# Kernel optimization log

Hardware: AMD Instinct MI355X
Metric: run time of the kernel (lower is better)

## Reference

```python
import jax, jax.numpy as jnp
import numpy as np

D, J, K, H = 4, 256, 512, 512  # d, num_output, num_input, num_hidden
B = 1024


def setup_inputs() -> dict:
    key = jax.random.key(0)
    ks = jax.random.split(key, 8)
    x = jax.random.normal(ks[0], (B, K), dtype=jnp.float32)
    # self.w = ((1-0.1)*U + 0.1) / num_input, shape [d, num_output, num_input]
    w = ((0.9 * jax.random.uniform(ks[1], (D, J, K), dtype=jnp.float32) + 0.1) / K)
    # Stacked per-output-MLP params (nn.Linear default init scale 1/sqrt(fan_in))
    s0 = 1.0 / np.sqrt(K)
    s1 = 1.0 / np.sqrt(H)
    W0 = jax.random.uniform(ks[2], (J, H, K), dtype=jnp.float32, minval=-s0, maxval=s0)
    b0 = jax.random.uniform(ks[3], (J, H), dtype=jnp.float32, minval=-s0, maxval=s0)
    W1 = jax.random.uniform(ks[4], (J, H), dtype=jnp.float32, minval=-s1, maxval=s1)  # [J,1,H] squeezed
    b1 = jax.random.uniform(ks[5], (J,), dtype=jnp.float32, minval=-s1, maxval=s1)
    logvar = jnp.ones((D,), dtype=jnp.float32) * -4.0
    return {"x": x, "i": 0, "w": w, "W0": W0, "b0": b0, "W1": W1, "b1": b1, "logvar": logvar}


def reference(x, i, w, W0, b0, W1, b1, logvar):
    # For each output j: mu[:, j] = lin1_j(LeakyReLU(lin0_j(w[i, j] * x)))
    # Fused as a single grouped GEMM over j: fold the mask w[i] into the contraction.
    wi = w[i]                                   # [J, K]
    h = jnp.einsum('jhk,jk,bk->bjh', W0, wi, x) + b0[None, :, :]   # [B, J, H]
    h = jax.nn.leaky_relu(h, negative_slope=0.01)
    mu = jnp.einsum('bjh,jh->bj', h, W1) + b1[None, :]             # [B, J]
    return (mu, logvar)
```

## Files before the change

kernel.cpp:

```cpp
#include <hip/hip_runtime.h>

#define J_ 256
#define K_ 512
#define H_ 512
#define B_ 1024

typedef float f32x4 __attribute__((ext_vector_type(4)));
typedef unsigned int u32x4 __attribute__((ext_vector_type(4)));
typedef unsigned short u16x4 __attribute__((ext_vector_type(4)));
typedef unsigned short u16x8 __attribute__((ext_vector_type(8)));
typedef __bf16 bf16x8 __attribute__((ext_vector_type(8)));

__device__ __forceinline__ unsigned short f2bf(float f) {
    unsigned int u = __float_as_uint(f);
    u += 0x7fffu + ((u >> 16) & 1u);
    return (unsigned short)(u >> 16);
}

__device__ __forceinline__ void gload_lds16(const void* g, void* l) {
    __builtin_amdgcn_global_load_lds(
        (const __attribute__((address_space(1))) unsigned int*)g,
        (__attribute__((address_space(3))) unsigned int*)l, 16, 0, 0);
}

__global__ __launch_bounds__(256) void prep_kernel(
    const float* __restrict__ x, const float* __restrict__ b1,
    const float* __restrict__ logvar, unsigned short* __restrict__ xbf,
    float* __restrict__ out) {
    int t = blockIdx.x * 256 + threadIdx.x;
    {
        f32x4 v = *(const f32x4*)(x + (size_t)t * 4);
        u16x4 o;
        o[0] = f2bf(v[0]); o[1] = f2bf(v[1]); o[2] = f2bf(v[2]); o[3] = f2bf(v[3]);
        *(u16x4*)(xbf + (size_t)t * 4) = o;
    }
    if (t < (B_ * J_) / 4) {
        int b = t >> 6;
        int j4 = (t & 63) << 2;
        f32x4 bb = *(const f32x4*)(b1 + j4);
        *(f32x4*)(out + ((size_t)b << 8) + j4) = bb;
    }
    if (t < 4) out[B_ * J_ + t] = logvar[t];
}

__global__ __launch_bounds__(256) void wprep_kernel(
    const float* __restrict__ W0, const float* __restrict__ wmask,
    const int* __restrict__ ip, unsigned short* __restrict__ w0p) {
    size_t t = (size_t)blockIdx.x * 256 + threadIdx.x;
    size_t e = t * 8;
    int j = (int)(e >> 18);
    int k = (int)(e & (K_ - 1));
    const float* wi = wmask + ((size_t)ip[0] * J_ + j) * K_ + k;
    f32x4 s0 = *(const f32x4*)wi;
    f32x4 s1 = *(const f32x4*)(wi + 4);
    f32x4 a0 = *(const f32x4*)(W0 + e);
    f32x4 a1 = *(const f32x4*)(W0 + e + 4);
    a0 *= s0; a1 *= s1;
    u16x8 o;
    #pragma unroll
    for (int q = 0; q < 4; ++q) { o[q] = f2bf(a0[q]); o[q + 4] = f2bf(a1[q]); }
    *(u16x8*)(w0p + e) = o;
}

__global__ __launch_bounds__(512, 1) void enc_kernel(
    const unsigned short* __restrict__ xbf,
    const unsigned short* __restrict__ w0p,
    const float* __restrict__ b0,
    const float* __restrict__ W1,
    float* __restrict__ out) {
    __shared__ unsigned char lds[3 * 49152];

    int p = blockIdx.x;
    int xcd = p & 7;
    int q = p >> 3;
    int j = (xcd << 5) + (q >> 4);
    int inner = q & 15;
    int m0 = (inner >> 2) << 8;
    int h0 = (inner & 3) << 7;

    int tid = threadIdx.x;
    int lane = tid & 63;
    int wv = tid >> 6;
    int wmv = wv >> 1;
    int wnv = wv & 1;
    int lr = lane & 15, lg = lane >> 4;

    int lrow = lane >> 3;
    int lch = lane & 7;
    int sch = ((lch ^ lrow) << 3);

    const unsigned short* aSrc = xbf + (size_t)(m0 + wv * 8 + lrow) * K_ + sch;
    const unsigned short* bSrc = w0p + ((size_t)j * H_ + h0 + wv * 8 + lrow) * K_ + sch;
    unsigned char* ldsAW = lds + wv * 1024;
    unsigned char* ldsBW = lds + 32768 + wv * 1024;

    f32x4 acc[4][4] = {};

#define VMW(n) do { asm volatile("s_waitcnt vmcnt(" #n ")" ::: "memory"); \
                    __builtin_amdgcn_sched_barrier(0); } while (0)
#define BAR() do { __builtin_amdgcn_s_barrier(); \
                   __builtin_amdgcn_sched_barrier(0); } while (0)

#define STAGE(bi, ks) do { \
    _Pragma("unroll") for (int ii = 0; ii < 4; ++ii) \
        gload_lds16(aSrc + (size_t)ii * 64 * K_ + (ks) * 64, \
                    ldsAW + (bi) * 49152 + ii * 8192); \
    _Pragma("unroll") for (int ii = 0; ii < 2; ++ii) \
        gload_lds16(bSrc + (size_t)ii * 64 * K_ + (ks) * 64, \
                    ldsBW + (bi) * 49152 + ii * 8192); \
    } while (0)

#define COMPUTE(bi) do { \
    const unsigned char* LA = lds + (bi) * 49152; \
    const unsigned char* LB = LA + 32768; \
    _Pragma("unroll") for (int kf = 0; kf < 2; ++kf) { \
        bf16x8 af[4], bv[4]; \
        int colk = (kf << 6) + (lg << 4); \
        _Pragma("unroll") for (int mf = 0; mf < 4; ++mf) { \
            int r = (wmv << 6) + (mf << 4) + lr; \
            af[mf] = *(const bf16x8*)(LA + r * 128 + (colk ^ ((r & 7) << 4))); \
        } \
        _Pragma("unroll") for (int nf = 0; nf < 4; ++nf) { \
            int hr = (wnv << 6) + (nf << 4) + lr; \
            bv[nf] = *(const bf16x8*)(LB + hr * 128 + (colk ^ ((hr & 7) << 4))); \
        } \
        __builtin_amdgcn_s_setprio(1); \
        _Pragma("unroll") for (int mf = 0; mf < 4; ++mf) \
            _Pragma("unroll") for (int nf = 0; nf < 4; ++nf) \
                acc[mf][nf] = __builtin_amdgcn_mfma_f32_16x16x32_bf16( \
                    af[mf], bv[nf], acc[mf][nf], 0, 0, 0); \
        __builtin_amdgcn_s_setprio(0); \
    } } while (0)

    STAGE(0, 0); STAGE(1, 1);
    STAGE(2, 2); VMW(12); BAR(); COMPUTE(0); BAR();
    STAGE(0, 3); VMW(12); BAR(); COMPUTE(1); BAR();
    STAGE(1, 4); VMW(12); BAR(); COMPUTE(2); BAR();
    STAGE(2, 5); VMW(12); BAR(); COMPUTE(0); BAR();
    STAGE(0, 6); VMW(12); BAR(); COMPUTE(1); BAR();
    STAGE(1, 7); VMW(12); BAR(); COMPUTE(2); BAR();
                 VMW(6);  BAR(); COMPUTE(0); BAR();
                 VMW(0);  BAR(); COMPUTE(1);

    float b0v[4], w1v[4];
    #pragma unroll
    for (int nf = 0; nf < 4; ++nf) {
        int col = h0 + (wnv << 6) + (nf << 4) + lr;
        b0v[nf] = b0[(size_t)j * H_ + col];
        w1v[nf] = W1[(size_t)j * H_ + col];
    }
    #pragma unroll
    for (int mf = 0; mf < 4; ++mf) {
        #pragma unroll
        for (int rg = 0; rg < 4; ++rg) {
            float ps = 0.f;
            #pragma unroll
            for (int nf = 0; nf < 4; ++nf) {
                float hv = acc[mf][nf][rg] + b0v[nf];
                hv = hv > 0.f ? hv : 0.01f * hv;
                ps += hv * w1v[nf];
            }
            ps += __shfl_xor(ps, 1);
            ps += __shfl_xor(ps, 2);
            ps += __shfl_xor(ps, 4);
            ps += __shfl_xor(ps, 8);
            if (lr == 0) {
                int row = m0 + (wmv << 6) + (mf << 4) + (lg << 2) + rg;
                atomicAdd(out + (size_t)row * J_ + j, ps);
            }
        }
    }
#undef VMW
#undef BAR
#undef STAGE
#undef COMPUTE
}

__global__ __launch_bounds__(256, 2) void enc_kernel_fb(
    const unsigned short* __restrict__ xbf,
    const float* __restrict__ W0,
    const float* __restrict__ wmask,
    const int* __restrict__ ip,
    const float* __restrict__ b0,
    const float* __restrict__ W1,
    float* __restrict__ out) {
    __shared__ unsigned char ldsA[128 * 128];
    __shared__ unsigned char ldsB[128 * 128];

    int p = blockIdx.x;
    int xcd = p & 7;
    int q = p >> 3;
    int j = (xcd << 5) + (q >> 5);
    int inner = q & 31;
    int m0 = (inner >> 2) << 7;
    int h0 = (inner & 3) << 7;

    int i = ip[0];
    const float* w0j = W0 + (size_t)j * (H_ * K_);
    const float* wij = wmask + ((size_t)i * J_ + j) * K_;

    int tid = threadIdx.x;
    int lane = tid & 63;
    int wv = tid >> 6;
    int wm = wv >> 1, wn = wv & 1;
    int lr = lane & 15, lg = lane >> 4;
    int srow0 = tid >> 3;
    int c = tid & 7;

    f32x4 acc[4][4] = {};

    for (int ks = 0; ks < K_ / 64; ++ks) {
        int k0 = ks * 64;
        #pragma unroll
        for (int it = 0; it < 4; ++it) {
            int r = srow0 + it * 32;
            u32x4 v = *(const u32x4*)(xbf + (size_t)(m0 + r) * K_ + k0 + c * 8);
            *(u32x4*)(ldsA + r * 128 + ((c * 16) ^ ((r & 7) << 4))) = v;
        }
        f32x4 s0 = *(const f32x4*)(wij + k0 + c * 8);
        f32x4 s1 = *(const f32x4*)(wij + k0 + c * 8 + 4);
        #pragma unroll
        for (int it = 0; it < 4; ++it) {
            int hr = srow0 + it * 32;
            const float* src = w0j + (size_t)(h0 + hr) * K_ + k0 + c * 8;
            f32x4 a0 = *(const f32x4*)(src);
            f32x4 a1 = *(const f32x4*)(src + 4);
            a0 *= s0; a1 *= s1;
            u16x8 bvv;
            #pragma unroll
            for (int e = 0; e < 4; ++e) { bvv[e] = f2bf(a0[e]); bvv[e + 4] = f2bf(a1[e]); }
            *(u16x8*)(ldsB + hr * 128 + ((c * 16) ^ ((hr & 7) << 4))) = bvv;
        }
        __syncthreads();
        #pragma unroll
        for (int kf = 0; kf < 2; ++kf) {
            bf16x8 af[4], bfr[4];
            #pragma unroll
            for (int mf = 0; mf < 4; ++mf) {
                int r = (wm << 6) + (mf << 4) + lr;
                af[mf] = *(const bf16x8*)(ldsA + r * 128 +
                          (((kf << 6) + (lg << 4)) ^ ((r & 7) << 4)));
            }
            #pragma unroll
            for (int nf = 0; nf < 4; ++nf) {
                int hrw = (wn << 6) + (nf << 4) + lr;
                bfr[nf] = *(const bf16x8*)(ldsB + hrw * 128 +
                          (((kf << 6) + (lg << 4)) ^ ((hrw & 7) << 4)));
            }
            #pragma unroll
            for (int mf = 0; mf < 4; ++mf)
                #pragma unroll
                for (int nf = 0; nf < 4; ++nf)
                    acc[mf][nf] = __builtin_amdgcn_mfma_f32_16x16x32_bf16(
                        af[mf], bfr[nf], acc[mf][nf], 0, 0, 0);
        }
        __syncthreads();
    }

    float b0v[4], w1v[4];
    #pragma unroll
    for (int nf = 0; nf < 4; ++nf) {
        int h = h0 + (wn << 6) + (nf << 4) + lr;
        b0v[nf] = b0[(size_t)j * H_ + h];
        w1v[nf] = W1[(size_t)j * H_ + h];
    }
    #pragma unroll
    for (int mf = 0; mf < 4; ++mf) {
        #pragma unroll
        for (int rg = 0; rg < 4; ++rg) {
            float ps = 0.f;
            #pragma unroll
            for (int nf = 0; nf < 4; ++nf) {
                float hv = acc[mf][nf][rg] + b0v[nf];
                hv = hv > 0.f ? hv : 0.01f * hv;
                ps += hv * w1v[nf];
            }
            ps += __shfl_xor(ps, 1);
            ps += __shfl_xor(ps, 2);
            ps += __shfl_xor(ps, 4);
            ps += __shfl_xor(ps, 8);
            if (lr == 0) {
                int row = m0 + (wm << 6) + (mf << 4) + (lg << 2) + rg;
                atomicAdd(out + (size_t)row * J_ + j, ps);
            }
        }
    }
}

extern "C" void kernel_launch(void* const* d_in, const int* in_sizes, int n_in,
                              void* d_out, int out_size, void* d_ws, size_t ws_size,
                              hipStream_t stream) {
    const float* x      = (const float*)d_in[0];
    const int*   ip     = (const int*)d_in[1];
    const float* wmask  = (const float*)d_in[2];
    const float* W0     = (const float*)d_in[3];
    const float* b0     = (const float*)d_in[4];
    const float* W1     = (const float*)d_in[5];
    const float* b1     = (const float*)d_in[6];
    const float* logvar = (const float*)d_in[7];
    float* out = (float*)d_out;
    unsigned short* xbf = (unsigned short*)d_ws;
    const size_t xbf_elems = (size_t)B_ * K_;
    const size_t w0p_bytes = (size_t)J_ * H_ * K_ * 2;
    const size_t need = xbf_elems * 2 + w0p_bytes;

    prep_kernel<<<512, 256, 0, stream>>>(x, b1, logvar, xbf, out);
    if (ws_size >= need) {
        unsigned short* w0p = xbf + xbf_elems;
        wprep_kernel<<<32768, 256, 0, stream>>>(W0, wmask, ip, w0p);
        enc_kernel<<<4096, 512, 0, stream>>>(xbf, w0p, b0, W1, out);
    } else {
        enc_kernel_fb<<<8192, 256, 0, stream>>>(xbf, W0, wmask, ip, b0, W1, out);
    }
}
```

Before: 587.0 us.

## Enlarge GEMM tile to 256x256 with 4-stage K32 pipeline and register prefetch

Restructures the grouped GEMM kernel so each block computes a 256x256 tile (8 waves arranged 2x4) instead of 256x128, halving the grid. It also cuts the K-step to 32 with a 4-deep LDS ring (128 KB instead of 144 KB) and a new swizzle. LDS fragments for the next step are prefetched into registers while MFMAs run, and the A and B staging loads are split around mid-iteration barriers. The larger tile raises arithmetic intensity and halves the atomic partial sums, but it doubles accumulator registers and requests 2 blocks per CU, which may not fit in LDS and can cause register spills.

After: 596.3 us. No clear change (+1.6%).

```diff
diff --git a/kernel.cpp b/kernel.cpp
--- a/kernel.cpp
+++ b/kernel.cpp
@@ -62,85 +62,102 @@
     *(u16x8*)(w0p + e) = o;
 }
 
-__global__ __launch_bounds__(512, 1) void enc_kernel(
+__global__ __launch_bounds__(512, 2) void enc_kernel(
     const unsigned short* __restrict__ xbf,
     const unsigned short* __restrict__ w0p,
     const float* __restrict__ b0,
     const float* __restrict__ W1,
     float* __restrict__ out) {
-    __shared__ unsigned char lds[3 * 49152];
+    __shared__ unsigned char ldsA[4 * 16384];
+    __shared__ unsigned char ldsB[4 * 16384];
 
     int p = blockIdx.x;
     int xcd = p & 7;
-    int q = p >> 3;
-    int j = (xcd << 5) + (q >> 4);
-    int inner = q & 15;
-    int m0 = (inner >> 2) << 8;
-    int h0 = (inner & 3) << 7;
+    int t = p >> 3;
+    int j = (xcd << 5) + (t >> 3);
+    int inner = t & 7;
+    int m0 = (inner >> 1) << 8;
+    int h0 = (inner & 1) << 8;
 
     int tid = threadIdx.x;
     int lane = tid & 63;
     int wv = tid >> 6;
-    int wmv = wv >> 1;
-    int wnv = wv & 1;
+    int wmv = wv >> 2;
+    int wnv = wv & 3;
     int lr = lane & 15, lg = lane >> 4;
 
-    int lrow = lane >> 3;
-    int lch = lane & 7;
-    int sch = ((lch ^ lrow) << 3);
-
-    const unsigned short* aSrc = xbf + (size_t)(m0 + wv * 8 + lrow) * K_ + sch;
-    const unsigned short* bSrc = w0p + ((size_t)j * H_ + h0 + wv * 8 + lrow) * K_ + sch;
-    unsigned char* ldsAW = lds + wv * 1024;
-    unsigned char* ldsBW = lds + 32768 + wv * 1024;
-
-    f32x4 acc[4][4] = {};
+    int sRow = lane >> 2;
+    int sChk = lane & 3;
+    int srcChunk = sChk ^ ((lane >> 3) & 3);
+
+    const unsigned short* aSrc = xbf + (size_t)(m0 + wv * 16 + sRow) * K_ + srcChunk * 8;
+    const unsigned short* bSrc = w0p + ((size_t)j * H_ + h0 + wv * 16 + sRow) * K_ + srcChunk * 8;
+    unsigned char* ldsAw = ldsA + wv * 1024;
+    unsigned char* ldsBw = ldsB + wv * 1024;
+
+    int fx = (lg ^ ((lr >> 1) & 3)) << 4;
+    const unsigned char* aF = ldsA + (wmv * 128 + lr) * 64 + fx;
+    const unsigned char* bF = ldsB + (wnv * 64 + lr) * 64 + fx;
+
+    f32x4 acc[8][4] = {};
 
 #define VMW(n) do { asm volatile("s_waitcnt vmcnt(" #n ")" ::: "memory"); \
                     __builtin_amdgcn_sched_barrier(0); } while (0)
+#define LGKM0() do { asm volatile("s_waitcnt lgkmcnt(0)" ::: "memory"); \
+                     __builtin_amdgcn_sched_barrier(0); } while (0)
 #define BAR() do { __builtin_amdgcn_s_barrier(); \
                    __builtin_amdgcn_sched_barrier(0); } while (0)
-
-#define STAGE(bi, ks) do { \
-    _Pragma("unroll") for (int ii = 0; ii < 4; ++ii) \
-        gload_lds16(aSrc + (size_t)ii * 64 * K_ + (ks) * 64, \
-                    ldsAW + (bi) * 49152 + ii * 8192); \
-    _Pragma("unroll") for (int ii = 0; ii < 2; ++ii) \
-        gload_lds16(bSrc + (size_t)ii * 64 * K_ + (ks) * 64, \
-                    ldsBW + (bi) * 49152 + ii * 8192); \
-    } while (0)
-
-#define COMPUTE(bi) do { \
-    const unsigned char* LA = lds + (bi) * 49152; \
-    const unsigned char* LB = LA + 32768; \
-    _Pragma("unroll") for (int kf = 0; kf < 2; ++kf) { \
-        bf16x8 af[4], bv[4]; \
-        int colk = (kf << 6) + (lg << 4); \
-        _Pragma("unroll") for (int mf = 0; mf < 4; ++mf) { \
-            int r = (wmv << 6) + (mf << 4) + lr; \
-            af[mf] = *(const bf16x8*)(LA + r * 128 + (colk ^ ((r & 7) << 4))); \
-        } \
-        _Pragma("unroll") for (int nf = 0; nf < 4; ++nf) { \
-            int hr = (wnv << 6) + (nf << 4) + lr; \
-            bv[nf] = *(const bf16x8*)(LB + hr * 128 + (colk ^ ((hr & 7) << 4))); \
-        } \
-        __builtin_amdgcn_s_setprio(1); \
-        _Pragma("unroll") for (int mf = 0; mf < 4; ++mf) \
-            _Pragma("unroll") for (int nf = 0; nf < 4; ++nf) \
-                acc[mf][nf] = __builtin_amdgcn_mfma_f32_16x16x32_bf16( \
-                    af[mf], bv[nf], acc[mf][nf], 0, 0, 0); \
-        __builtin_amdgcn_s_setprio(0); \
-    } } while (0)
-
-    STAGE(0, 0); STAGE(1, 1);
-    STAGE(2, 2); VMW(12); BAR(); COMPUTE(0); BAR();
-    STAGE(0, 3); VMW(12); BAR(); COMPUTE(1); BAR();
-    STAGE(1, 4); VMW(12); BAR(); COMPUTE(2); BAR();
-    STAGE(2, 5); VMW(12); BAR(); COMPUTE(0); BAR();
-    STAGE(0, 6); VMW(12); BAR(); COMPUTE(1); BAR();
-    STAGE(1, 7); VMW(12); BAR(); COMPUTE(2); BAR();
-                 VMW(6);  BAR(); COMPUTE(0); BAR();
-                 VMW(0);  BAR(); COMPUTE(1);
+#define STG_A(tt) do { int c_ = (tt) & 3; \
+    gload_lds16(aSrc + (tt) * 32,                      ldsAw + c_ * 16384); \
+    gload_lds16(aSrc + (tt) * 32 + (size_t)128 * K_,   ldsAw + c_ * 16384 + 8192); } while (0)
+#define STG_B(tt) do { int c_ = (tt) & 3; \
+    gload_lds16(bSrc + (tt) * 32,                      ldsBw + c_ * 16384); \
+    gload_lds16(bSrc + (tt) * 32 + (size_t)128 * K_,   ldsBw + c_ * 16384 + 8192); } while (0)
+#define LD_A(dst, tt, mf) (dst) = *(const bf16x8*)(aF + ((tt) & 3) * 16384 + (mf) * 1024)
+#define LD_B(dst, tt, nf) (dst) = *(const bf16x8*)(bF + ((tt) & 3) * 16384 + (nf) * 1024)
+#define MFMAQ(mq, ar) do { __builtin_amdgcn_s_setprio(1); \
+    _Pragma("unroll") for (int nf_ = 0; nf_ < 4; ++nf_) { \
+      _Pragma("unroll") for (int mf_ = 0; mf_ < 4; ++mf_) \
+        acc[(mq) * 4 + mf_][nf_] = __builtin_amdgcn_mfma_f32_16x16x32_bf16( \
+            ar[mf_], bC[nf_], acc[(mq) * 4 + mf_][nf_], 0, 0, 0); } \
+    __builtin_amdgcn_s_setprio(0); } while (0)
+
+    STG_A(0); STG_B(0); STG_A(1); STG_B(1); STG_A(2); STG_B(2);
+    VMW(8);
+    BAR();
+
+    bf16x8 aLo[4], bC[4];
+    LD_A(aLo[0], 0, 0); LD_A(aLo[1], 0, 1); LD_A(aLo[2], 0, 2); LD_A(aLo[3], 0, 3);
+    LD_B(bC[0], 0, 0);  LD_B(bC[1], 0, 1);  LD_B(bC[2], 0, 2);  LD_B(bC[3], 0, 3);
+
+    #pragma unroll
+    for (int kt = 0; kt < 16; ++kt) {
+        if (kt <= 12) STG_A(kt + 3);
+        bf16x8 aHi[4];
+        LD_A(aHi[0], kt, 4); LD_A(aHi[1], kt, 5);
+        LD_A(aHi[2], kt, 6); LD_A(aHi[3], kt, 7);
+        MFMAQ(0, aLo);
+        LGKM0();
+        if (kt <= 12)      { VMW(6); }
+        else if (kt == 13) { VMW(4); }
+        else if (kt == 14) { VMW(0); }
+        BAR();
+        if (kt <= 12) STG_B(kt + 3);
+        bf16x8 aN[4], bN[4];
+        if (kt < 15) {
+            LD_A(aN[0], kt + 1, 0); LD_A(aN[1], kt + 1, 1);
+            LD_A(aN[2], kt + 1, 2); LD_A(aN[3], kt + 1, 3);
+            LD_B(bN[0], kt + 1, 0); LD_B(bN[1], kt + 1, 1);
+            LD_B(bN[2], kt + 1, 2); LD_B(bN[3], kt + 1, 3);
+        }
+        MFMAQ(1, aHi);
+        if (kt < 15) {
+            LGKM0();
+            BAR();
+            aLo[0] = aN[0]; aLo[1] = aN[1]; aLo[2] = aN[2]; aLo[3] = aN[3];
+            bC[0] = bN[0];  bC[1] = bN[1];  bC[2] = bN[2];  bC[3] = bN[3];
+        }
+    }
 
     float b0v[4], w1v[4];
     #pragma unroll
@@ -150,7 +167,7 @@
         w1v[nf] = W1[(size_t)j * H_ + col];
     }
     #pragma unroll
-    for (int mf = 0; mf < 4; ++mf) {
+    for (int mf = 0; mf < 8; ++mf) {
         #pragma unroll
         for (int rg = 0; rg < 4; ++rg) {
             float ps = 0.f;
@@ -165,15 +182,19 @@
             ps += __shfl_xor(ps, 4);
             ps += __shfl_xor(ps, 8);
             if (lr == 0) {
-                int row = m0 + (wmv << 6) + (mf << 4) + (lg << 2) + rg;
+                int row = m0 + (wmv << 7) + (mf << 4) + (lg << 2) + rg;
                 atomicAdd(out + (size_t)row * J_ + j, ps);
             }
         }
     }
 #undef VMW
+#undef LGKM0
 #undef BAR
-#undef STAGE
-#undef COMPUTE
+#undef STG_A
+#undef STG_B
+#undef LD_A
+#undef LD_B
+#undef MFMAQ
 }
 
 __global__ __launch_bounds__(256, 2) void enc_kernel_fb(
@@ -308,7 +329,7 @@
     if (ws_size >= need) {
         unsigned short* w0p = xbf + xbf_elems;
         wprep_kernel<<<32768, 256, 0, stream>>>(W0, wmask, ip, w0p);
-        enc_kernel<<<4096, 512, 0, stream>>>(xbf, w0p, b0, W1, out);
+        enc_kernel<<<2048, 512, 0, stream>>>(xbf, w0p, b0, W1, out);
     } else {
         enc_kernel_fb<<<8192, 256, 0, stream>>>(xbf, W0, wmask, ip, b0, W1, out);
     }
```
